# Kernel optimization log

Measured on AMD Instinct MI355X. Metric: run time of the kernel, lower is better.

The kernel has to match this reference:

```python
import jax, jax.numpy as jnp
import numpy as np
from math import sqrt

BS, SEQ, NV, DM, K = 16, 1024, 512, 256, 8
EPS = 0.05  # sinkhorn epsilon
TEMP = 0.07  # concrete-bernoulli temperature


def setup_inputs() -> dict:
    key = jax.random.key(0)
    k1, k2, k3 = jax.random.split(key, 3)
    x = jax.random.normal(k1, (BS, SEQ, NV), jnp.float32)
    # nn.Linear(seq_len, d_model): weight [d_model, seq_len], bias [d_model]
    W = jax.random.normal(k2, (DM, SEQ), jnp.float32) / sqrt(SEQ)
    b = jnp.zeros((DM,), jnp.float32)
    cluster_emb = jax.random.normal(k3, (K, DM), jnp.float32) / sqrt(DM)
    return {"x": x, "W": W, "b": b, "cluster_emb": cluster_emb}


def _l2norm(z):
    # F.normalize(x, dim=1, p=2) with eps=1e-12 clamp
    n = jnp.maximum(jnp.linalg.norm(z, axis=1, keepdims=True), 1e-12)
    return z / n


def _sinkhorn(q):
    Q = jnp.exp(q / EPS)
    return Q / jnp.sum(Q, axis=1, keepdims=True)


def _concrete_bern(p, key):
    u = jax.random.uniform(key, p.shape, p.dtype, 1e-10, 1.0 - 1e-10)
    noise = jnp.log(u) - jnp.log1p(-u)
    logit = jnp.log(p + 1e-10) - jnp.log(1.0 - p + 1e-10)
    return jax.nn.sigmoid((logit + noise) / TEMP)


def _forward(x, W, b, cluster_emb):
    bs, S, nv = x.shape
    d = W.shape[0]
    k = cluster_emb.shape[0]
    # permute -> [bs, nv, S], Linear(S -> d)
    x_emb = jnp.einsum('bsv,ds->bvd', x, W) + b  # [bs, nv, d]
    x_flat = x_emb.reshape(-1, d)  # [bs*nv, d]
    # cosine-similarity cluster logits
    prob = (_l2norm(x_flat) @ _l2norm(cluster_emb).T).reshape(bs, nv, k)
    prob_temp = _sinkhorn(prob.reshape(-1, k)).reshape(bs, nv, k)  # individual probs
    prob_avg = _sinkhorn(jnp.mean(prob, axis=0))  # [nv, k]
    mask = _concrete_bern(prob_avg, jax.random.key(42))  # [nv, k]
    # CrossAttention with n_heads=1 (dropout inactive in eval)
    scale = 1.0 / sqrt(d)
    scores = jnp.einsum('kd,bvd->bkv', cluster_emb, x_emb)  # [bs, k, nv]
    A = jax.nn.softmax(scale * scores, axis=-1) * mask.T[None]  # masked attn
    V = jnp.einsum('bkv,bvd->bkd', A, x_emb)  # [bs, k, d]
    cluster_emb_avg = jnp.mean(V, axis=0)  # [k, d] (stored attribute in torch)
    # cluster_base_encoding: straight-through bernoulli, broadcast over seq_len
    soft = prob_temp.transpose(2, 0, 1)[..., None]  # [k, bs, nv, 1]
    u = jax.random.uniform(jax.random.key(7), soft.shape, soft.dtype)
    bern = (u < jax.lax.stop_gradient(soft)).astype(soft.dtype)
    extend = jnp.broadcast_to(bern, (k, bs, nv, S))  # [k, bs, nv, S]
    hard = soft + jax.lax.stop_gradient(extend - soft)  # straight-through
    return hard


def reference(x, W, b, cluster_emb):
    return _forward(x, W, b, cluster_emb)
```

## Files before the change

kernel.cpp:

```cpp
#include <hip/hip_runtime.h>
#include <math.h>
#include <stdint.h>

#define BS 16
#define SEQ 1024
#define NV 512
#define DM 256
#define NK 8

typedef __attribute__((ext_vector_type(8))) short bf16x8;
typedef __attribute__((ext_vector_type(4))) float f32x4;

__device__ double g_WC[NK * SEQ];
__device__ double g_Bk[NK];
__device__ __align__(16) unsigned short g_x0[BS * NV * SEQ];
__device__ __align__(16) unsigned short g_x1[BS * NV * SEQ];
__device__ __align__(16) unsigned short g_x2[BS * NV * SEQ];
__device__ __align__(16) unsigned short g_w0[DM * SEQ];
__device__ __align__(16) unsigned short g_w1[DM * SEQ];
__device__ __align__(16) unsigned short g_w2[DM * SEQ];
__device__ double g_nn2p[2][BS * NV];
__device__ double g_Dp[8 * BS * NV * NK];
__device__ unsigned char g_bits[BS * NV];

__device__ __forceinline__ void threefry2x32_key7(uint32_t x0, uint32_t x1,
                                                  uint32_t& o0, uint32_t& o1) {
    const uint32_t k0 = 0u, k1 = 7u;
    const uint32_t k2 = k0 ^ k1 ^ 0x1BD11BDAu;
    uint32_t v0 = x0 + k0, v1 = x1 + k1;
#define TF_ROUND(r) { v0 += v1; v1 = (v1 << (r)) | (v1 >> (32 - (r))); v1 ^= v0; }
    TF_ROUND(13) TF_ROUND(15) TF_ROUND(26) TF_ROUND(6)
    v0 += k1; v1 += k2 + 1u;
    TF_ROUND(17) TF_ROUND(29) TF_ROUND(16) TF_ROUND(24)
    v0 += k2; v1 += k0 + 2u;
    TF_ROUND(13) TF_ROUND(15) TF_ROUND(26) TF_ROUND(6)
    v0 += k0; v1 += k1 + 3u;
    TF_ROUND(17) TF_ROUND(29) TF_ROUND(16) TF_ROUND(24)
    v0 += k1; v1 += k2 + 4u;
    TF_ROUND(13) TF_ROUND(15) TF_ROUND(26) TF_ROUND(6)
    v0 += k2; v1 += k0 + 5u;
#undef TF_ROUND
    o0 = v0; o1 = v1;
}

__device__ __forceinline__ float bits_to_uniform(uint32_t b) {
    return __uint_as_float((b >> 9) | 0x3F800000u) - 1.0f;
}

__device__ __forceinline__ unsigned short f2bf(float f) {
    uint32_t u = __float_as_uint(f);
    return (unsigned short)((u + 0x7FFFu + ((u >> 16) & 1u)) >> 16);
}
__device__ __forceinline__ float bf2f(unsigned short h) {
    return __uint_as_float(((uint32_t)h) << 16);
}
__device__ __forceinline__ void split3(float f, unsigned short& h0,
                                       unsigned short& h1, unsigned short& h2) {
    h0 = f2bf(f);
    float r1 = f - bf2f(h0);
    h1 = f2bf(r1);
    float r2 = r1 - bf2f(h1);
    h2 = f2bf(r2);
}

__device__ __forceinline__ void cp16s(const unsigned short* g, unsigned short* l) {
    __builtin_amdgcn_global_load_lds(
        (const __attribute__((address_space(1))) void*)g,
        (__attribute__((address_space(3))) void*)l,
        16, 0, 0);
}

__global__ __launch_bounds__(256) void prep_kernel(
        const float* __restrict__ W, const float* __restrict__ bias,
        const float* __restrict__ ce) {
    __shared__ double red[256];
    __shared__ double cen[256];
    const int t = threadIdx.x;
    const int bid = blockIdx.x;

    if (bid >= 32) {
        const int base = (bid - 32) * 4096 + t * 16;
        uint32_t p0[8], p1[8], p2[8];
#pragma unroll
        for (int i = 0; i < 16; ++i) {
            unsigned short h0, h1, h2;
            split3(W[base + i], h0, h1, h2);
            if (i & 1) {
                p0[i >> 1] |= (uint32_t)h0 << 16;
                p1[i >> 1] |= (uint32_t)h1 << 16;
                p2[i >> 1] |= (uint32_t)h2 << 16;
            } else {
                p0[i >> 1] = h0; p1[i >> 1] = h1; p2[i >> 1] = h2;
            }
        }
        *(uint4*)&g_w0[base]     = make_uint4(p0[0], p0[1], p0[2], p0[3]);
        *(uint4*)&g_w0[base + 8] = make_uint4(p0[4], p0[5], p0[6], p0[7]);
        *(uint4*)&g_w1[base]     = make_uint4(p1[0], p1[1], p1[2], p1[3]);
        *(uint4*)&g_w1[base + 8] = make_uint4(p1[4], p1[5], p1[6], p1[7]);
        *(uint4*)&g_w2[base]     = make_uint4(p2[0], p2[1], p2[2], p2[3]);
        *(uint4*)&g_w2[base + 8] = make_uint4(p2[4], p2[5], p2[6], p2[7]);
        return;
    }

    const int k = bid >> 2;
    const int schunk = bid & 3;

    double c = (double)ce[k * DM + t];
    red[t] = c * c;
    __syncthreads();
    for (int off = 128; off > 0; off >>= 1) {
        if (t < off) red[t] += red[t + off];
        __syncthreads();
    }
    double nc = fmax(sqrt(red[0]), 1e-12);
    cen[t] = c / nc;
    __syncthreads();
    red[t] = (double)bias[t] * cen[t];
    __syncthreads();
    for (int off = 128; off > 0; off >>= 1) {
        if (t < off) red[t] += red[t + off];
        __syncthreads();
    }
    if (t == 0 && schunk == 0) g_Bk[k] = red[0];

    const int s = schunk * 256 + t;
    double acc = 0.0;
#pragma unroll 8
    for (int d = 0; d < DM; ++d)
        acc += cen[d] * (double)W[(size_t)d * SEQ + s];
    g_WC[(size_t)k * SEQ + s] = acc;
}

__global__ __launch_bounds__(256) void xsplit_kernel(const float* __restrict__ x) {
    __shared__ float tile[64][65];
    const int t = threadIdx.x;
    const int stile = blockIdx.x >> 3, vtile = blockIdx.x & 7;
    const int b = blockIdx.y;
    const int s0 = stile * 64, v0 = vtile * 64;
    const float* xb = x + ((size_t)b * SEQ + s0) * NV + v0;

#pragma unroll
    for (int p = 0; p < 16; ++p) {
        int lin = p * 256 + t;
        int sl = lin >> 6, vv = lin & 63;
        tile[sl][vv] = xb[(size_t)sl * NV + vv];
    }
    __syncthreads();

    const int vr = t >> 2, g = t & 3;
    const size_t obase = ((size_t)b * NV + v0 + vr) * SEQ + s0 + g * 16;
    uint32_t p0[8], p1[8], p2[8];
#pragma unroll
    for (int i = 0; i < 16; ++i) {
        unsigned short h0, h1, h2;
        split3(tile[g * 16 + i][vr], h0, h1, h2);
        if (i & 1) {
            p0[i >> 1] |= (uint32_t)h0 << 16;
            p1[i >> 1] |= (uint32_t)h1 << 16;
            p2[i >> 1] |= (uint32_t)h2 << 16;
        } else {
            p0[i >> 1] = h0; p1[i >> 1] = h1; p2[i >> 1] = h2;
        }
    }
    *(uint4*)&g_x0[obase]     = make_uint4(p0[0], p0[1], p0[2], p0[3]);
    *(uint4*)&g_x0[obase + 8] = make_uint4(p0[4], p0[5], p0[6], p0[7]);
    *(uint4*)&g_x1[obase]     = make_uint4(p1[0], p1[1], p1[2], p1[3]);
    *(uint4*)&g_x1[obase + 8] = make_uint4(p1[4], p1[5], p1[6], p1[7]);
    *(uint4*)&g_x2[obase]     = make_uint4(p2[0], p2[1], p2[2], p2[3]);
    *(uint4*)&g_x2[obase + 8] = make_uint4(p2[4], p2[5], p2[6], p2[7]);
}

#define KC 32

__global__ __launch_bounds__(256) void gemm_kernel(const float* __restrict__ bias) {
    __shared__ __align__(16) unsigned short xs[2][3][32 * 32];
    __shared__ __align__(16) unsigned short ws[2][3][128 * 32];
    __shared__ double dred[4][32];

    const int t = threadIdx.x;
    const int dblk = blockIdx.x;
    const int vt   = blockIdx.y;
    const int b    = blockIdx.z;
    const int v0 = vt * 32, d0 = dblk * 128;
    const int w = t >> 6, l = t & 63;

    const int srow = l >> 2;
    const int sk8  = ((l & 3) ^ ((l >> 2) & 3)) * 8;
    const int rrow = l & 15;
    const int rsl  = ((l >> 4) ^ (l & 3)) * 8;

    const size_t xbase = ((size_t)b * NV + v0) * SEQ;
    const size_t wbase = (size_t)d0 * SEQ;
    const unsigned short* xsrc[3] = {g_x0 + xbase, g_x1 + xbase, g_x2 + xbase};
    const unsigned short* wsrc[3] = {g_w0 + wbase, g_w1 + wbase, g_w2 + wbase};

    f32x4 acc[2][2];
    double zac[2][2][4];
#pragma unroll
    for (int mb = 0; mb < 2; ++mb)
#pragma unroll
        for (int nb = 0; nb < 2; ++nb) {
            acc[mb][nb] = (f32x4){0.f, 0.f, 0.f, 0.f};
#pragma unroll
            for (int r = 0; r < 4; ++r) zac[mb][nb][r] = 0.0;
        }

#define STAGE(BUF, C)                                                          \
    {                                                                          \
        const int S0 = (C) * KC;                                               \
        _Pragma("unroll")                                                      \
        for (int sp = 0; sp < 3; ++sp) {                                       \
            cp16s(&wsrc[sp][(size_t)(w * 32 + srow) * SEQ + S0 + sk8],         \
                  &ws[BUF][sp][(w * 32) * 32]);                                \
            cp16s(&wsrc[sp][(size_t)(w * 32 + 16 + srow) * SEQ + S0 + sk8],    \
                  &ws[BUF][sp][(w * 32 + 16) * 32]);                           \
        }                                                                      \
        if (w < 3) {                                                           \
            cp16s(&xsrc[w][(size_t)srow * SEQ + S0 + sk8], &xs[BUF][w][0]);    \
            cp16s(&xsrc[w][(size_t)(16 + srow) * SEQ + S0 + sk8],              \
                  &xs[BUF][w][16 * 32]);                                       \
        }                                                                      \
    }

    STAGE(0, 0)
    __syncthreads();

    for (int c = 0; c < 32; ++c) {
        const int buf = c & 1;
        if (c < 31) STAGE(buf ^ 1, c + 1)

        bf16x8 a[3][2], bb[3][2];
#pragma unroll
        for (int sp = 0; sp < 3; ++sp) {
#pragma unroll
            for (int mb = 0; mb < 2; ++mb)
                a[sp][mb] = *(const bf16x8*)&xs[buf][sp][(mb * 16 + rrow) * 32 + rsl];
#pragma unroll
            for (int nb = 0; nb < 2; ++nb)
                bb[sp][nb] = *(const bf16x8*)
                    &ws[buf][sp][(w * 32 + nb * 16 + rrow) * 32 + rsl];
        }
#pragma unroll
        for (int mb = 0; mb < 2; ++mb)
#pragma unroll
            for (int nb = 0; nb < 2; ++nb) {
                f32x4 v = acc[mb][nb];
                v = __builtin_amdgcn_mfma_f32_16x16x32_bf16(a[1][mb], bb[1][nb], v, 0, 0, 0);
                v = __builtin_amdgcn_mfma_f32_16x16x32_bf16(a[0][mb], bb[2][nb], v, 0, 0, 0);
                v = __builtin_amdgcn_mfma_f32_16x16x32_bf16(a[2][mb], bb[0][nb], v, 0, 0, 0);
                v = __builtin_amdgcn_mfma_f32_16x16x32_bf16(a[0][mb], bb[1][nb], v, 0, 0, 0);
                v = __builtin_amdgcn_mfma_f32_16x16x32_bf16(a[1][mb], bb[0][nb], v, 0, 0, 0);
                v = __builtin_amdgcn_mfma_f32_16x16x32_bf16(a[0][mb], bb[0][nb], v, 0, 0, 0);
                acc[mb][nb] = v;
            }

        if ((c & 7) == 7) {
#pragma unroll
            for (int mb = 0; mb < 2; ++mb)
#pragma unroll
                for (int nb = 0; nb < 2; ++nb) {
#pragma unroll
                    for (int r = 0; r < 4; ++r)
                        zac[mb][nb][r] += (double)acc[mb][nb][r];
                    acc[mb][nb] = (f32x4){0.f, 0.f, 0.f, 0.f};
                }
        }

        __syncthreads();
    }
#undef STAGE

    double sv[2][4];
#pragma unroll
    for (int mb = 0; mb < 2; ++mb)
#pragma unroll
        for (int r = 0; r < 4; ++r) sv[mb][r] = 0.0;
#pragma unroll
    for (int mb = 0; mb < 2; ++mb)
#pragma unroll
        for (int nb = 0; nb < 2; ++nb) {
            const int d = d0 + w * 32 + nb * 16 + (l & 15);
            const double bd = (double)bias[d];
#pragma unroll
            for (int r = 0; r < 4; ++r) {
                double z = zac[mb][nb][r] + bd;
                sv[mb][r] += z * z;
            }
        }
#pragma unroll
    for (int mb = 0; mb < 2; ++mb)
#pragma unroll
        for (int r = 0; r < 4; ++r) {
            double s = sv[mb][r];
            s += __shfl_xor(s, 1);
            s += __shfl_xor(s, 2);
            s += __shfl_xor(s, 4);
            s += __shfl_xor(s, 8);
            sv[mb][r] = s;
        }
    if ((l & 15) == 0) {
#pragma unroll
        for (int mb = 0; mb < 2; ++mb)
#pragma unroll
            for (int r = 0; r < 4; ++r)
                dred[w][mb * 16 + (l >> 4) * 4 + r] = sv[mb][r];
    }
    __syncthreads();
    if (t < 32) {
        double s = dred[0][t] + dred[1][t] + dred[2][t] + dred[3][t];
        g_nn2p[dblk][b * NV + v0 + t] = s;
    }
}

__global__ __launch_bounds__(256) void dkern(const float* __restrict__ x) {
    __shared__ double wcd[NK][128];
    __shared__ double dw[4][64][NK];
    const int t = threadIdx.x;
    const int vblk = blockIdx.x;
    const int b    = blockIdx.y;
    const int sc   = blockIdx.z;
    const int v0 = vblk * 64;
    const int ss = sc * 128;

#pragma unroll
    for (int j = 0; j < 4; ++j) {
        int idx = j * 256 + t;
        ((double*)wcd)[idx] = g_WC[(size_t)(idx >> 7) * SEQ + ss + (idx & 127)];
    }
    __syncthreads();

    const int vl = t & 63, w = t >> 6;
    const float* xp = x + (size_t)b * SEQ * NV + v0 + vl;
    double D[NK];
#pragma unroll
    for (int k = 0; k < NK; ++k) D[k] = 0.0;
    const int sw = w * 32;
    for (int i = 0; i < 32; ++i) {
        int sl = sw + i;
        double xv = (double)xp[(size_t)(ss + sl) * NV];
#pragma unroll
        for (int k = 0; k < NK; ++k) D[k] += xv * wcd[k][sl];
    }
#pragma unroll
    for (int k = 0; k < NK; ++k) dw[w][vl][k] = D[k];
    __syncthreads();

    const int v = t & 63, k2 = (t >> 6) * 2;
#pragma unroll
    for (int j = 0; j < 2; ++j) {
        int k = k2 + j;
        double s = dw[0][v][k] + dw[1][v][k] + dw[2][v][k] + dw[3][v][k];
        g_Dp[(((size_t)sc * BS + b) * NV + v0 + v) * NK + k] = s;
    }
}

__global__ __launch_bounds__(256) void finalize_kernel() {
    const int bv = blockIdx.x * 256 + threadIdx.x;
    double n = fmax(sqrt(g_nn2p[0][bv] + g_nn2p[1][bv]), 1e-12);

    double D[NK];
#pragma unroll
    for (int k = 0; k < NK; ++k) D[k] = g_Bk[k];
#pragma unroll
    for (int sc = 0; sc < 8; ++sc) {
#pragma unroll
        for (int k = 0; k < NK; ++k)
            D[k] += g_Dp[((size_t)sc * (BS * NV) + bv) * NK + k];
    }

    double p[NK], sum = 0.0;
#pragma unroll
    for (int k = 0; k < NK; ++k) {
        p[k] = exp((D[k] / n) / 0.05);
        sum += p[k];
    }
    unsigned int byte = 0;
#pragma unroll
    for (int k = 0; k < NK; ++k) {
        uint32_t i = (uint32_t)(k * (BS * NV) + bv);
        uint32_t y0, y1;
        threefry2x32_key7(0u, i, y0, y1);
        float u = bits_to_uniform(y0 ^ y1);
        if ((double)u < p[k] / sum) byte |= 1u << k;
    }
    g_bits[bv] = (unsigned char)byte;
}

__global__ __launch_bounds__(256) void write_kernel(float* __restrict__ out) {
    const int t = threadIdx.x;
    const size_t r0 = (size_t)blockIdx.x * 8;
#pragma unroll
    for (int j = 0; j < 8; ++j) {
        size_t r = r0 + j;
        unsigned int bv = (unsigned int)(r & 8191u);
        unsigned int k  = (unsigned int)(r >> 13);
        float v = ((g_bits[bv] >> k) & 1u) ? 1.0f : 0.0f;
        float4 val = make_float4(v, v, v, v);
        ((float4*)(out + r * 1024))[t] = val;
    }
}

extern "C" void kernel_launch(void* const* d_in, const int* in_sizes, int n_in,
                              void* d_out, int out_size, void* d_ws, size_t ws_size,
                              hipStream_t stream) {
    const float* x    = (const float*)d_in[0];
    const float* W    = (const float*)d_in[1];
    const float* bias = (const float*)d_in[2];
    const float* ce   = (const float*)d_in[3];
    float* out = (float*)d_out;

    prep_kernel<<<dim3(96), dim3(256), 0, stream>>>(W, bias, ce);
    xsplit_kernel<<<dim3(128, 16), dim3(256), 0, stream>>>(x);
    gemm_kernel<<<dim3(2, 16, 16), dim3(256), 0, stream>>>(bias);
    dkern<<<dim3(8, 16, 8), dim3(256), 0, stream>>>(x);
    finalize_kernel<<<dim3(32), dim3(256), 0, stream>>>();
    write_kernel<<<dim3(8192), dim3(256), 0, stream>>>(out);
}
```

Before: 396.4 us.

## Pre-tile split bf16 operands into MFMA fragment layout and load directly from global

The prep and xsplit kernels now write the three bf16 splits of W and x in a tiled layout where each 16-row by 32-k chunk is stored exactly as the MFMA lanes consume it. The GEMM kernel drops its LDS double-buffer staging and per-chunk barriers and instead has each lane read its bf16x8 fragments straight from global memory with contiguous 16-byte loads. This removes the LDS traffic and synchronisation cost. In exchange, fragments shared across waves are fetched separately by each wave through the caches, and there is no explicit prefetch to hide global latency.

```diff
diff --git a/kernel.cpp b/kernel.cpp
--- a/kernel.cpp
+++ b/kernel.cpp
@@ -63,13 +63,6 @@
     h2 = f2bf(r2);
 }
 
-__device__ __forceinline__ void cp16s(const unsigned short* g, unsigned short* l) {
-    __builtin_amdgcn_global_load_lds(
-        (const __attribute__((address_space(1))) void*)g,
-        (__attribute__((address_space(3))) void*)l,
-        16, 0, 0);
-}
-
 __global__ __launch_bounds__(256) void prep_kernel(
         const float* __restrict__ W, const float* __restrict__ bias,
         const float* __restrict__ ce) {
@@ -80,6 +73,10 @@
 
     if (bid >= 32) {
         const int base = (bid - 32) * 4096 + t * 16;
+        const int d = base >> 10, s = base & 1023;
+        const int dt = d >> 4, row = d & 15;
+        const int kc = s >> 5, kslot = (s >> 3) & 3;
+        const size_t off0 = ((((size_t)dt * 32 + kc) * 64) + (row | (kslot << 4))) * 8;
         uint32_t p0[8], p1[8], p2[8];
 #pragma unroll
         for (int i = 0; i < 16; ++i) {
@@ -93,12 +90,12 @@
                 p0[i >> 1] = h0; p1[i >> 1] = h1; p2[i >> 1] = h2;
             }
         }
-        *(uint4*)&g_w0[base]     = make_uint4(p0[0], p0[1], p0[2], p0[3]);
-        *(uint4*)&g_w0[base + 8] = make_uint4(p0[4], p0[5], p0[6], p0[7]);
-        *(uint4*)&g_w1[base]     = make_uint4(p1[0], p1[1], p1[2], p1[3]);
-        *(uint4*)&g_w1[base + 8] = make_uint4(p1[4], p1[5], p1[6], p1[7]);
-        *(uint4*)&g_w2[base]     = make_uint4(p2[0], p2[1], p2[2], p2[3]);
-        *(uint4*)&g_w2[base + 8] = make_uint4(p2[4], p2[5], p2[6], p2[7]);
+        *(uint4*)&g_w0[off0]       = make_uint4(p0[0], p0[1], p0[2], p0[3]);
+        *(uint4*)&g_w0[off0 + 128] = make_uint4(p0[4], p0[5], p0[6], p0[7]);
+        *(uint4*)&g_w1[off0]       = make_uint4(p1[0], p1[1], p1[2], p1[3]);
+        *(uint4*)&g_w1[off0 + 128] = make_uint4(p1[4], p1[5], p1[6], p1[7]);
+        *(uint4*)&g_w2[off0]       = make_uint4(p2[0], p2[1], p2[2], p2[3]);
+        *(uint4*)&g_w2[off0 + 128] = make_uint4(p2[4], p2[5], p2[6], p2[7]);
         return;
     }
 
@@ -147,8 +144,14 @@
     }
     __syncthreads();
 
-    const int vr = t >> 2, g = t & 3;
-    const size_t obase = ((size_t)b * NV + v0 + vr) * SEQ + s0 + g * 16;
+    const int vr = t & 63, g = t >> 6;
+    const int v = v0 + vr;
+    const int s8 = s0 + g * 16;
+    const int vt = v >> 4, row = v & 15;
+    const int kc = s8 >> 5, kslot = (s8 >> 3) & 3;
+    const size_t off0 =
+        ((((size_t)b * 32 + vt) * 32 + kc) * 64 + (row | (kslot << 4))) * 8;
+
     uint32_t p0[8], p1[8], p2[8];
 #pragma unroll
     for (int i = 0; i < 16; ++i) {
@@ -162,37 +165,42 @@
             p0[i >> 1] = h0; p1[i >> 1] = h1; p2[i >> 1] = h2;
         }
     }
-    *(uint4*)&g_x0[obase]     = make_uint4(p0[0], p0[1], p0[2], p0[3]);
-    *(uint4*)&g_x0[obase + 8] = make_uint4(p0[4], p0[5], p0[6], p0[7]);
-    *(uint4*)&g_x1[obase]     = make_uint4(p1[0], p1[1], p1[2], p1[3]);
-    *(uint4*)&g_x1[obase + 8] = make_uint4(p1[4], p1[5], p1[6], p1[7]);
-    *(uint4*)&g_x2[obase]     = make_uint4(p2[0], p2[1], p2[2], p2[3]);
-    *(uint4*)&g_x2[obase + 8] = make_uint4(p2[4], p2[5], p2[6], p2[7]);
-}
-
-#define KC 32
+    *(uint4*)&g_x0[off0]       = make_uint4(p0[0], p0[1], p0[2], p0[3]);
+    *(uint4*)&g_x0[off0 + 128] = make_uint4(p0[4], p0[5], p0[6], p0[7]);
+    *(uint4*)&g_x1[off0]       = make_uint4(p1[0], p1[1], p1[2], p1[3]);
+    *(uint4*)&g_x1[off0 + 128] = make_uint4(p1[4], p1[5], p1[6], p1[7]);
+    *(uint4*)&g_x2[off0]       = make_uint4(p2[0], p2[1], p2[2], p2[3]);
+    *(uint4*)&g_x2[off0 + 128] = make_uint4(p2[4], p2[5], p2[6], p2[7]);
+}
 
 __global__ __launch_bounds__(256) void gemm_kernel(const float* __restrict__ bias) {
-    __shared__ __align__(16) unsigned short xs[2][3][32 * 32];
-    __shared__ __align__(16) unsigned short ws[2][3][128 * 32];
     __shared__ double dred[4][32];
 
     const int t = threadIdx.x;
     const int dblk = blockIdx.x;
     const int vt   = blockIdx.y;
     const int b    = blockIdx.z;
-    const int v0 = vt * 32, d0 = dblk * 128;
+    const int d0 = dblk * 128;
+    const int v0 = vt * 32;
     const int w = t >> 6, l = t & 63;
 
-    const int srow = l >> 2;
-    const int sk8  = ((l & 3) ^ ((l >> 2) & 3)) * 8;
-    const int rrow = l & 15;
-    const int rsl  = ((l >> 4) ^ (l & 3)) * 8;
-
-    const size_t xbase = ((size_t)b * NV + v0) * SEQ;
-    const size_t wbase = (size_t)d0 * SEQ;
-    const unsigned short* xsrc[3] = {g_x0 + xbase, g_x1 + xbase, g_x2 + xbase};
-    const unsigned short* wsrc[3] = {g_w0 + wbase, g_w1 + wbase, g_w2 + wbase};
+    const unsigned short* pa[3][2];
+    const unsigned short* pb[3][2];
+    {
+        const unsigned short* xa[3] = {g_x0, g_x1, g_x2};
+        const unsigned short* wa[3] = {g_w0, g_w1, g_w2};
+#pragma unroll
+        for (int sp = 0; sp < 3; ++sp) {
+#pragma unroll
+            for (int mb = 0; mb < 2; ++mb)
+                pa[sp][mb] = xa[sp] +
+                    ((((size_t)b * 32 + vt * 2 + mb) * 32) * 64 + l) * 8;
+#pragma unroll
+            for (int nb = 0; nb < 2; ++nb)
+                pb[sp][nb] = wa[sp] +
+                    (((size_t)(dblk * 8 + w * 2 + nb) * 32) * 64 + l) * 8;
+        }
+    }
 
     f32x4 acc[2][2];
     double zac[2][2][4];
@@ -205,70 +213,46 @@
             for (int r = 0; r < 4; ++r) zac[mb][nb][r] = 0.0;
         }
 
-#define STAGE(BUF, C)                                                          \
-    {                                                                          \
-        const int S0 = (C) * KC;                                               \
-        _Pragma("unroll")                                                      \
-        for (int sp = 0; sp < 3; ++sp) {                                       \
-            cp16s(&wsrc[sp][(size_t)(w * 32 + srow) * SEQ + S0 + sk8],         \
-                  &ws[BUF][sp][(w * 32) * 32]);                                \
-            cp16s(&wsrc[sp][(size_t)(w * 32 + 16 + srow) * SEQ + S0 + sk8],    \
-                  &ws[BUF][sp][(w * 32 + 16) * 32]);                           \
-        }                                                                      \
-        if (w < 3) {                                                           \
-            cp16s(&xsrc[w][(size_t)srow * SEQ + S0 + sk8], &xs[BUF][w][0]);    \
-            cp16s(&xsrc[w][(size_t)(16 + srow) * SEQ + S0 + sk8],              \
-                  &xs[BUF][w][16 * 32]);                                       \
-        }                                                                      \
-    }
-
-    STAGE(0, 0)
-    __syncthreads();
-
-    for (int c = 0; c < 32; ++c) {
-        const int buf = c & 1;
-        if (c < 31) STAGE(buf ^ 1, c + 1)
-
-        bf16x8 a[3][2], bb[3][2];
-#pragma unroll
-        for (int sp = 0; sp < 3; ++sp) {
+    for (int q = 0; q < 4; ++q) {
+        for (int c8 = 0; c8 < 8; ++c8) {
+            bf16x8 a[3][2], bb[3][2];
+#pragma unroll
+            for (int sp = 0; sp < 3; ++sp) {
+#pragma unroll
+                for (int mb = 0; mb < 2; ++mb) {
+                    a[sp][mb] = *(const bf16x8*)pa[sp][mb];
+                    pa[sp][mb] += 512;
+                }
+#pragma unroll
+                for (int nb = 0; nb < 2; ++nb) {
+                    bb[sp][nb] = *(const bf16x8*)pb[sp][nb];
+                    pb[sp][nb] += 512;
+                }
+            }
 #pragma unroll
             for (int mb = 0; mb < 2; ++mb)
-                a[sp][mb] = *(const bf16x8*)&xs[buf][sp][(mb * 16 + rrow) * 32 + rsl];
-#pragma unroll
-            for (int nb = 0; nb < 2; ++nb)
-                bb[sp][nb] = *(const bf16x8*)
-                    &ws[buf][sp][(w * 32 + nb * 16 + rrow) * 32 + rsl];
+#pragma unroll
+                for (int nb = 0; nb < 2; ++nb) {
+                    f32x4 v = acc[mb][nb];
+                    v = __builtin_amdgcn_mfma_f32_16x16x32_bf16(a[1][mb], bb[1][nb], v, 0, 0, 0);
+                    v = __builtin_amdgcn_mfma_f32_16x16x32_bf16(a[0][mb], bb[2][nb], v, 0, 0, 0);
+                    v = __builtin_amdgcn_mfma_f32_16x16x32_bf16(a[2][mb], bb[0][nb], v, 0, 0, 0);
+                    v = __builtin_amdgcn_mfma_f32_16x16x32_bf16(a[0][mb], bb[1][nb], v, 0, 0, 0);
+                    v = __builtin_amdgcn_mfma_f32_16x16x32_bf16(a[1][mb], bb[0][nb], v, 0, 0, 0);
+                    v = __builtin_amdgcn_mfma_f32_16x16x32_bf16(a[0][mb], bb[0][nb], v, 0, 0, 0);
+                    acc[mb][nb] = v;
+                }
         }
 #pragma unroll
         for (int mb = 0; mb < 2; ++mb)
 #pragma unroll
             for (int nb = 0; nb < 2; ++nb) {
-                f32x4 v = acc[mb][nb];
-                v = __builtin_amdgcn_mfma_f32_16x16x32_bf16(a[1][mb], bb[1][nb], v, 0, 0, 0);
-                v = __builtin_amdgcn_mfma_f32_16x16x32_bf16(a[0][mb], bb[2][nb], v, 0, 0, 0);
-                v = __builtin_amdgcn_mfma_f32_16x16x32_bf16(a[2][mb], bb[0][nb], v, 0, 0, 0);
-                v = __builtin_amdgcn_mfma_f32_16x16x32_bf16(a[0][mb], bb[1][nb], v, 0, 0, 0);
-                v = __builtin_amdgcn_mfma_f32_16x16x32_bf16(a[1][mb], bb[0][nb], v, 0, 0, 0);
-                v = __builtin_amdgcn_mfma_f32_16x16x32_bf16(a[0][mb], bb[0][nb], v, 0, 0, 0);
-                acc[mb][nb] = v;
+#pragma unroll
+                for (int r = 0; r < 4; ++r)
+                    zac[mb][nb][r] += (double)acc[mb][nb][r];
+                acc[mb][nb] = (f32x4){0.f, 0.f, 0.f, 0.f};
             }
-
-        if ((c & 7) == 7) {
-#pragma unroll
-            for (int mb = 0; mb < 2; ++mb)
-#pragma unroll
-                for (int nb = 0; nb < 2; ++nb) {
-#pragma unroll
-                    for (int r = 0; r < 4; ++r)
-                        zac[mb][nb][r] += (double)acc[mb][nb][r];
-                    acc[mb][nb] = (f32x4){0.f, 0.f, 0.f, 0.f};
-                }
-        }
-
-        __syncthreads();
-    }
-#undef STAGE
+    }
 
     double sv[2][4];
 #pragma unroll
```

New measurement: 368.5 us. 7.0% less time.
